# Optimization experiments

Measured on AMD Instinct MI355X. Metric: run time of the kernel, lower is better.

## Reference

```python
import jax, jax.numpy as jnp
import numpy as np

NUM_GRAPHS = 32

def leaky(x):
    return jax.nn.leaky_relu(x, 0.1)

def setup_inputs() -> dict:
    key = jax.random.key(0)
    ks = jax.random.split(key, 32)
    N, E = 8000, 32000
    x = jax.random.normal(ks[0], (N, 4), dtype=jnp.float32)
    edge_index = jax.random.randint(ks[1], (2, E), 0, N, dtype=jnp.int32)
    batch_index = jnp.sort(jax.random.randint(ks[2], (N,), 0, NUM_GRAPHS, dtype=jnp.int32))
    def lin(k, i, o, s=0.1):
        k1, k2 = jax.random.split(k)
        return jax.random.normal(k1, (i, o), dtype=jnp.float32) * s, jax.random.normal(k2, (o,), dtype=jnp.float32) * s
    p = {}
    # edge networks: Linear(3,64)+LeakyReLU+Linear(64, in*out)+LeakyReLU
    p['en1_w1'], p['en1_b1'] = lin(ks[3], 3, 64)
    p['en1_w2'], p['en1_b2'] = lin(ks[4], 64, 4 * 8)
    p['en2_w1'], p['en2_b1'] = lin(ks[5], 3, 64)
    p['en2_w2'], p['en2_b2'] = lin(ks[6], 64, 8 * 64)
    p['en3_w1'], p['en3_b1'] = lin(ks[7], 3, 64)
    p['en3_w2'], p['en3_b2'] = lin(ks[8], 64, 64 * 128)
    # NNConv root weights + biases
    p['root1'], p['cb1'] = lin(ks[9], 4, 8)
    p['root2'], p['cb2'] = lin(ks[10], 8, 64)
    p['root3'], p['cb3'] = lin(ks[11], 64, 128)
    # readout MLP
    p['fc1_w'], p['fc1_b'] = lin(ks[12], 128, 128)
    p['fc2_w'], p['fc2_b'] = lin(ks[13], 128, 64)
    p['fc3_w'], p['fc3_b'] = lin(ks[14], 64, 1)
    return dict(x=x, edge_index=edge_index, batch_index=batch_index, **p)

def nnconv(h, edge_index, edge_attr, w1, b1, w2, b2, root, cbias, in_ch, out_ch):
    # per-edge weight matrix from edge attributes
    e = leaky(edge_attr @ w1 + b1)              # [E,64]
    W = leaky(e @ w2 + b2).reshape(-1, in_ch, out_ch)  # [E,in,out]
    msg = jnp.einsum('ei,eio->eo', h[edge_index[0]], W)  # gather + per-edge matmul
    agg = jax.ops.segment_sum(msg, edge_index[1], num_segments=h.shape[0])  # scatter-add
    return agg + h @ root + cbias

def reference(x, edge_index, batch_index, en1_w1, en1_b1, en1_w2, en1_b2, en2_w1, en2_b1, en2_w2, en2_b2, en3_w1, en3_b1, en3_w2, en3_b2, root1, cb1, root2, cb2, root3, cb3, fc1_w, fc1_b, fc2_w, fc2_b, fc3_w, fc3_b):
    edge_attr = (x[edge_index[1]] - x[edge_index[0]])[:, 1:]  # [E,3] relative position
    h = leaky(nnconv(x, edge_index, edge_attr, en1_w1, en1_b1, en1_w2, en1_b2, root1, cb1, 4, 8))
    h = leaky(nnconv(h, edge_index, edge_attr, en2_w1, en2_b1, en2_w2, en2_b2, root2, cb2, 8, 64))
    h = leaky(nnconv(h, edge_index, edge_attr, en3_w1, en3_b1, en3_w2, en3_b2, root3, cb3, 64, 128))
    g = jax.ops.segment_sum(h, batch_index, num_segments=NUM_GRAPHS)  # sum-pool per graph
    g = leaky(g @ fc1_w + fc1_b)
    g = leaky(g @ fc2_w + fc2_b)
    return g @ fc3_w + fc3_b  # [G,1] total energies
```

## Files before the change

### kernel.cpp

```cpp
#include <hip/hip_runtime.h>
#include <hip/hip_bf16.h>

typedef __attribute__((ext_vector_type(8))) short short8;
typedef __attribute__((ext_vector_type(4))) float floatx4;

__device__ __forceinline__ float leaky(float v){ return v > 0.f ? v : 0.1f*v; }
__device__ __forceinline__ void atomAdd(float* p, float v){ unsafeAtomicAdd(p, v); }
__device__ __forceinline__ short f2bf(float f){
  __hip_bfloat16 h = __float2bfloat16(f);
  return *reinterpret_cast<short*>(&h);
}

__global__ void efeat_all(const float* __restrict__ x, const int* __restrict__ ei,
                          const float* __restrict__ w1a, const float* __restrict__ b1a,
                          const float* __restrict__ w1b, const float* __restrict__ b1b,
                          const float* __restrict__ w1c, const float* __restrict__ b1c,
                          float* __restrict__ ef1, short* __restrict__ ef2b,
                          short* __restrict__ ef3b, int E, int Epad){
  int id = blockIdx.x*256 + threadIdx.x;
  if (id >= Epad*64) return;
  int e = id >> 6, j = id & 63;
  if (e >= E){ ef1[id] = 0.f; ef2b[id] = 0; ef3b[id] = 0; return; }
  int s = ei[e], d = ei[E+e];
  float a0 = x[d*4+1] - x[s*4+1];
  float a1 = x[d*4+2] - x[s*4+2];
  float a2 = x[d*4+3] - x[s*4+3];
  float v1 = leaky(a0*w1a[j] + a1*w1a[64+j] + a2*w1a[128+j] + b1a[j]);
  float v2 = leaky(a0*w1b[j] + a1*w1b[64+j] + a2*w1b[128+j] + b1b[j]);
  float v3 = leaky(a0*w1c[j] + a1*w1c[64+j] + a2*w1c[128+j] + b1c[j]);
  ef1[id] = v1;
  ef2b[id] = f2bf(v2);
  ef3b[id] = f2bf(v3);
}

__global__ void pack_w2_all(const float* __restrict__ w2a, short* __restrict__ pa,
                            const float* __restrict__ w2b, short* __restrict__ pb){
  int bid = blockIdx.x;
  const float* w2; short* dst; int IC, OC, cbase;
  if (bid < 16){ w2 = w2a; dst = pa; IC = 8;  OC = 64;  cbase = bid*4; }
  else        { w2 = w2b; dst = pb; IC = 64; OC = 128; cbase = (bid-16)*4; }
  int lane = threadIdx.x & 63;
  int c = cbase + (threadIdx.x >> 6);
  int OT = OC/16;
  int kh = c & 1; int rem = c >> 1; int otg = rem % OT; int i = rem / OT;
  int n = lane & 15, q = lane >> 4;
  short out[8];
  #pragma unroll
  for (int j=0;j<8;j++){
    int k = kh*32 + q*8 + j;
    out[j] = f2bf(w2[(size_t)k*(IC*OC) + i*OC + otg*16 + n]);
  }
  *reinterpret_cast<short8*>(dst + (size_t)c*512 + lane*8) = *reinterpret_cast<short8*>(out);
}

__global__ void conv1_kernel(const float* __restrict__ ef, const float* __restrict__ x,
                             const int* __restrict__ ei, const float* __restrict__ w2,
                             const float* __restrict__ b2, float* __restrict__ agg, int E){
  int id = blockIdx.x*256 + threadIdx.x;
  if (id >= E*8) return;
  int e = id >> 3, o = id & 7;
  int s = ei[e], d = ei[E+e];
  const float* efe = ef + (size_t)e*64;
  float z[4];
  #pragma unroll
  for (int i=0;i<4;i++) z[i] = b2[i*8+o];
  for (int k=0;k<64;k++){
    float a = efe[k];
    #pragma unroll
    for (int i=0;i<4;i++) z[i] += a*w2[k*32 + i*8 + o];
  }
  float msg = 0.f;
  #pragma unroll
  for (int i=0;i<4;i++) msg += x[s*4+i]*leaky(z[i]);
  atomAdd(&agg[d*8+o], msg);
}

template<int IC, int OC>
__global__ void node_kernel(float* __restrict__ h, const float* __restrict__ hin,
                            const float* __restrict__ root, const float* __restrict__ cb, int N){
  int id = blockIdx.x*256 + threadIdx.x;
  if (id >= N*OC) return;
  int n = id / OC, o = id % OC;
  float v = h[id] + cb[o];
  const float* hi = hin + (size_t)n*IC;
  #pragma unroll
  for (int i=0;i<IC;i++) v += hi[i]*root[i*OC+o];
  h[id] = leaky(v);
}

__global__ void node3_pool(const float* __restrict__ agg, const float* __restrict__ hin,
                           const float* __restrict__ root, const float* __restrict__ cb,
                           const int* __restrict__ batch, float* __restrict__ g, int N){
  int id = blockIdx.x*256 + threadIdx.x;
  if (id >= N*128) return;
  int n = id >> 7, o = id & 127;
  float v = agg[id] + cb[o];
  const float* hi = hin + (size_t)n*64;
  #pragma unroll
  for (int i=0;i<64;i++) v += hi[i]*root[i*128+o];
  atomAdd(&g[batch[n]*128 + o], leaky(v));
}

template<int IC, int OC, int MB, int ICB>
__global__ __launch_bounds__(256)
void conv_mfma(const short* __restrict__ efb, const float* __restrict__ h,
               const int* __restrict__ ei, const short* __restrict__ w2p,
               const float* __restrict__ b2, float* __restrict__ agg, int E){
  constexpr int ME   = MB*16;
  constexpr int OT   = OC/16;
  constexpr int WOT  = OT/4;
  constexpr int NSPL = IC/ICB;
  __shared__ float hsT[ICB][ME];
  __shared__ int sdst[ME];
  int tid = threadIdx.x;
  int bi = blockIdx.x;
  int eb = (bi / NSPL) * ME;
  int i0 = (bi % NSPL) * ICB;

  {
    int e = tid % ME;
    int ge = eb + e;
    bool valid = ge < E;
    int src = valid ? ei[ge] : 0;
    constexpr int CH  = 256/ME;
    constexpr int IPC = ICB/CH;
    int c = tid / ME;
    const float* hp = h + (size_t)src*IC + i0 + c*IPC;
    if constexpr (IPC == 8){
      #pragma unroll
      for (int half=0; half<2; half++){
        float4 hv = valid ? reinterpret_cast<const float4*>(hp)[half]
                          : float4{0.f,0.f,0.f,0.f};
        hsT[c*IPC + half*4 + 0][e] = hv.x;
        hsT[c*IPC + half*4 + 1][e] = hv.y;
        hsT[c*IPC + half*4 + 2][e] = hv.z;
        hsT[c*IPC + half*4 + 3][e] = hv.w;
      }
    } else {
      #pragma unroll
      for (int j=0;j<IPC;j++)
        hsT[c*IPC + j][e] = valid ? hp[j] : 0.f;
    }
    if (tid < ME) sdst[tid] = (eb + tid < E) ? ei[E + eb + tid] : -1;
  }
  __syncthreads();

  int lane = tid & 63;
  int wv = tid >> 6;
  int n = lane & 15, quad = lane >> 4;
  int o0 = wv * (OC/4);

  short8 A[MB][2];
  #pragma unroll
  for (int m=0;m<MB;m++)
    #pragma unroll
    for (int kh=0;kh<2;kh++)
      A[m][kh] = *reinterpret_cast<const short8*>(efb + (size_t)(eb + m*16 + n)*64 + kh*32 + quad*8);

  float msg[MB][WOT][4];
  #pragma unroll
  for (int m=0;m<MB;m++)
    #pragma unroll
    for (int t=0;t<WOT;t++)
      #pragma unroll
      for (int r=0;r<4;r++) msg[m][t][r] = 0.f;

  for (int i=0;i<ICB;i++){
    int ig = i0 + i;
    short8 B[WOT][2];
    float bz[WOT];
    #pragma unroll
    for (int t=0;t<WOT;t++){
      int otg = (o0 >> 4) + t;
      #pragma unroll
      for (int kh=0;kh<2;kh++)
        B[t][kh] = *reinterpret_cast<const short8*>(w2p + ((size_t)((ig*OT + otg)*2 + kh) << 9) + lane*8);
      bz[t] = b2[ig*OC + o0 + t*16 + n];
    }
    #pragma unroll
    for (int m=0;m<MB;m++){
      float4 hv = *reinterpret_cast<const float4*>(&hsT[i][m*16 + quad*4]);
      #pragma unroll
      for (int t=0;t<WOT;t++){
        floatx4 z = {bz[t], bz[t], bz[t], bz[t]};
        z = __builtin_amdgcn_mfma_f32_16x16x32_bf16(A[m][0], B[t][0], z, 0, 0, 0);
        z = __builtin_amdgcn_mfma_f32_16x16x32_bf16(A[m][1], B[t][1], z, 0, 0, 0);
        float l0 = fmaxf(z[0], 0.1f*z[0]);
        float l1 = fmaxf(z[1], 0.1f*z[1]);
        float l2 = fmaxf(z[2], 0.1f*z[2]);
        float l3 = fmaxf(z[3], 0.1f*z[3]);
        msg[m][t][0] += hv.x*l0;
        msg[m][t][1] += hv.y*l1;
        msg[m][t][2] += hv.z*l2;
        msg[m][t][3] += hv.w*l3;
      }
    }
  }

  #pragma unroll
  for (int m=0;m<MB;m++){
    #pragma unroll
    for (int r=0;r<4;r++){
      int d = sdst[m*16 + quad*4 + r];
      if (d >= 0){
        #pragma unroll
        for (int t=0;t<WOT;t++)
          atomAdd(&agg[(size_t)d*OC + o0 + t*16 + n], msg[m][t][r]);
      }
    }
  }
}

__global__ void head_kernel(const float* __restrict__ g,
                            const float* __restrict__ fc1w, const float* __restrict__ fc1b,
                            const float* __restrict__ fc2w, const float* __restrict__ fc2b,
                            const float* __restrict__ fc3w, const float* __restrict__ fc3b,
                            float* __restrict__ out){
  __shared__ float s1[128], s2[128];
  int gi = blockIdx.x, t = threadIdx.x;
  s1[t] = g[gi*128+t];
  __syncthreads();
  float v = fc1b[t];
  for (int i=0;i<128;i++) v += s1[i]*fc1w[i*128+t];
  s2[t] = leaky(v);
  __syncthreads();
  if (t < 64){
    float v2 = fc2b[t];
    for (int i=0;i<128;i++) v2 += s2[i]*fc2w[i*64+t];
    s1[t] = leaky(v2);
  }
  __syncthreads();
  if (t == 0){
    float v3 = fc3b[0];
    for (int i=0;i<64;i++) v3 += s1[i]*fc3w[i];
    out[gi] = v3;
  }
}

extern "C" void kernel_launch(void* const* d_in, const int* in_sizes, int n_in,
                              void* d_out, int out_size, void* d_ws, size_t ws_size,
                              hipStream_t stream) {
  const float* x      = (const float*)d_in[0];
  const int*   ei     = (const int*)  d_in[1];
  const int*   batch  = (const int*)  d_in[2];
  const float* en1_w1 = (const float*)d_in[3];  const float* en1_b1 = (const float*)d_in[4];
  const float* en1_w2 = (const float*)d_in[5];  const float* en1_b2 = (const float*)d_in[6];
  const float* en2_w1 = (const float*)d_in[7];  const float* en2_b1 = (const float*)d_in[8];
  const float* en2_w2 = (const float*)d_in[9];  const float* en2_b2 = (const float*)d_in[10];
  const float* en3_w1 = (const float*)d_in[11]; const float* en3_b1 = (const float*)d_in[12];
  const float* en3_w2 = (const float*)d_in[13]; const float* en3_b2 = (const float*)d_in[14];
  const float* root1  = (const float*)d_in[15]; const float* cb1    = (const float*)d_in[16];
  const float* root2  = (const float*)d_in[17]; const float* cb2    = (const float*)d_in[18];
  const float* root3  = (const float*)d_in[19]; const float* cb3    = (const float*)d_in[20];
  const float* fc1w   = (const float*)d_in[21]; const float* fc1b   = (const float*)d_in[22];
  const float* fc2w   = (const float*)d_in[23]; const float* fc2b   = (const float*)d_in[24];
  const float* fc3w   = (const float*)d_in[25]; const float* fc3b   = (const float*)d_in[26];
  float* out = (float*)d_out;

  const int N = in_sizes[0] / 4;
  const int E = in_sizes[1] / 2;
  const int G = 32;
  const int Epad = (E + 63) & ~63;

  float* ef1  = (float*)d_ws;
  short* ef2b = (short*)(ef1 + (size_t)Epad*64);
  short* ef3b = ef2b + (size_t)Epad*64;
  short* w2p2 = ef3b + (size_t)Epad*64;
  short* w2p3 = w2p2 + 8*4*2*512;
  float* a1   = (float*)(w2p3 + 64*8*2*512);
  float* a2   = a1 + (size_t)N*8;
  float* a3   = a2 + (size_t)N*64;
  float* g    = a3 + (size_t)N*128;

  size_t zero_bytes = ((size_t)N*(8+64+128) + (size_t)G*128) * sizeof(float);
  hipMemsetAsync(a1, 0, zero_bytes, stream);

  efeat_all<<<(Epad*64 + 255)/256, 256, 0, stream>>>(
      x, ei, en1_w1, en1_b1, en2_w1, en2_b1, en3_w1, en3_b1,
      ef1, ef2b, ef3b, E, Epad);

  pack_w2_all<<<272, 256, 0, stream>>>(en2_w2, w2p2, en3_w2, w2p3);

  conv1_kernel<<<(E*8 + 255)/256, 256, 0, stream>>>(ef1, x, ei, en1_w2, en1_b2, a1, E);
  node_kernel<4,8><<<(N*8 + 255)/256, 256, 0, stream>>>(a1, x, root1, cb1, N);

  conv_mfma<8,64,2,8><<<Epad/32, 256, 0, stream>>>(ef2b, a1, ei, w2p2, en2_b2, a2, E);
  node_kernel<8,64><<<(N*64 + 255)/256, 256, 0, stream>>>(a2, a1, root2, cb2, N);

  conv_mfma<64,128,4,32><<<(Epad/64)*2, 256, 0, stream>>>(ef3b, a2, ei, w2p3, en3_b2, a3, E);
  node3_pool<<<(N*128 + 255)/256, 256, 0, stream>>>(a3, a2, root3, cb3, batch, g, N);

  head_kernel<<<G, 128, 0, stream>>>(g, fc1w, fc1b, fc2w, fc2b, fc3w, fc3b, out);
}
```

Before: 254.1 us.

## Fuse conv1 into edge-feature kernel, tile node3 pool, prefetch B in conv_mfma

Merges the conv1 message computation into the edge-feature kernel, keeping layer-1 edge features in shared memory and dropping the fp32 ef1 buffer and one launch. node3_pool now stages root3 and 16 node rows in LDS and accumulates per-graph partial sums before issuing atomics, which cuts the number of global atomics. conv_mfma double-buffers the B-fragment loads across the input-channel loop so they overlap with the MFMA work. The fused conv1 leaves only 32 of 256 threads busy in its second phase, and each node3 block reloads the full 32KB root matrix.

```diff
diff --git a/kernel.cpp b/kernel.cpp
--- a/kernel.cpp
+++ b/kernel.cpp
@@ -11,26 +11,51 @@
   return *reinterpret_cast<short*>(&h);
 }
 
-__global__ void efeat_all(const float* __restrict__ x, const int* __restrict__ ei,
-                          const float* __restrict__ w1a, const float* __restrict__ b1a,
-                          const float* __restrict__ w1b, const float* __restrict__ b1b,
-                          const float* __restrict__ w1c, const float* __restrict__ b1c,
-                          float* __restrict__ ef1, short* __restrict__ ef2b,
-                          short* __restrict__ ef3b, int E, int Epad){
-  int id = blockIdx.x*256 + threadIdx.x;
-  if (id >= Epad*64) return;
+__global__ void efeat_conv1(const float* __restrict__ x, const int* __restrict__ ei,
+                            const float* __restrict__ w1a, const float* __restrict__ b1a,
+                            const float* __restrict__ w1b, const float* __restrict__ b1b,
+                            const float* __restrict__ w1c, const float* __restrict__ b1c,
+                            const float* __restrict__ c1w2, const float* __restrict__ c1b2,
+                            short* __restrict__ ef2b, short* __restrict__ ef3b,
+                            float* __restrict__ agg1, int E, int Epad){
+  __shared__ float sm[4][64];
+  int tid = threadIdx.x;
+  int id = blockIdx.x*256 + tid;
   int e = id >> 6, j = id & 63;
-  if (e >= E){ ef1[id] = 0.f; ef2b[id] = 0; ef3b[id] = 0; return; }
-  int s = ei[e], d = ei[E+e];
-  float a0 = x[d*4+1] - x[s*4+1];
-  float a1 = x[d*4+2] - x[s*4+2];
-  float a2 = x[d*4+3] - x[s*4+3];
-  float v1 = leaky(a0*w1a[j] + a1*w1a[64+j] + a2*w1a[128+j] + b1a[j]);
-  float v2 = leaky(a0*w1b[j] + a1*w1b[64+j] + a2*w1b[128+j] + b1b[j]);
-  float v3 = leaky(a0*w1c[j] + a1*w1c[64+j] + a2*w1c[128+j] + b1c[j]);
-  ef1[id] = v1;
-  ef2b[id] = f2bf(v2);
-  ef3b[id] = f2bf(v3);
+  float v1 = 0.f;
+  if (e < Epad){
+    if (e >= E){ ef2b[id] = 0; ef3b[id] = 0; }
+    else {
+      int s = ei[e], d = ei[E+e];
+      float a0 = x[d*4+1] - x[s*4+1];
+      float a1 = x[d*4+2] - x[s*4+2];
+      float a2 = x[d*4+3] - x[s*4+3];
+      v1 = leaky(a0*w1a[j] + a1*w1a[64+j] + a2*w1a[128+j] + b1a[j]);
+      ef2b[id] = f2bf(leaky(a0*w1b[j] + a1*w1b[64+j] + a2*w1b[128+j] + b1b[j]));
+      ef3b[id] = f2bf(leaky(a0*w1c[j] + a1*w1c[64+j] + a2*w1c[128+j] + b1c[j]));
+    }
+  }
+  sm[tid >> 6][j] = v1;
+  __syncthreads();
+  if (tid < 32){
+    int le = tid >> 3, o = tid & 7;
+    int ge = blockIdx.x*4 + le;
+    if (ge < E){
+      int s = ei[ge], d = ei[E+ge];
+      float z[4];
+      #pragma unroll
+      for (int i=0;i<4;i++) z[i] = c1b2[i*8+o];
+      for (int k=0;k<64;k++){
+        float a = sm[le][k];
+        #pragma unroll
+        for (int i=0;i<4;i++) z[i] += a*c1w2[k*32 + i*8 + o];
+      }
+      float msg = 0.f;
+      #pragma unroll
+      for (int i=0;i<4;i++) msg += x[s*4+i]*leaky(z[i]);
+      atomAdd(&agg1[d*8+o], msg);
+    }
+  }
 }
 
 __global__ void pack_w2_all(const float* __restrict__ w2a, short* __restrict__ pa,
@@ -53,28 +78,6 @@
   *reinterpret_cast<short8*>(dst + (size_t)c*512 + lane*8) = *reinterpret_cast<short8*>(out);
 }
 
-__global__ void conv1_kernel(const float* __restrict__ ef, const float* __restrict__ x,
-                             const int* __restrict__ ei, const float* __restrict__ w2,
-                             const float* __restrict__ b2, float* __restrict__ agg, int E){
-  int id = blockIdx.x*256 + threadIdx.x;
-  if (id >= E*8) return;
-  int e = id >> 3, o = id & 7;
-  int s = ei[e], d = ei[E+e];
-  const float* efe = ef + (size_t)e*64;
-  float z[4];
-  #pragma unroll
-  for (int i=0;i<4;i++) z[i] = b2[i*8+o];
-  for (int k=0;k<64;k++){
-    float a = efe[k];
-    #pragma unroll
-    for (int i=0;i<4;i++) z[i] += a*w2[k*32 + i*8 + o];
-  }
-  float msg = 0.f;
-  #pragma unroll
-  for (int i=0;i<4;i++) msg += x[s*4+i]*leaky(z[i]);
-  atomAdd(&agg[d*8+o], msg);
-}
-
 template<int IC, int OC>
 __global__ void node_kernel(float* __restrict__ h, const float* __restrict__ hin,
                             const float* __restrict__ root, const float* __restrict__ cb, int N){
@@ -88,17 +91,40 @@
   h[id] = leaky(v);
 }
 
-__global__ void node3_pool(const float* __restrict__ agg, const float* __restrict__ hin,
-                           const float* __restrict__ root, const float* __restrict__ cb,
-                           const int* __restrict__ batch, float* __restrict__ g, int N){
-  int id = blockIdx.x*256 + threadIdx.x;
-  if (id >= N*128) return;
-  int n = id >> 7, o = id & 127;
-  float v = agg[id] + cb[o];
-  const float* hi = hin + (size_t)n*64;
-  #pragma unroll
-  for (int i=0;i<64;i++) v += hi[i]*root[i*128+o];
-  atomAdd(&g[batch[n]*128 + o], leaky(v));
+__global__ __launch_bounds__(256)
+void node3_pool(const float* __restrict__ agg, const float* __restrict__ hin,
+                const float* __restrict__ root, const float* __restrict__ cb,
+                const int* __restrict__ batch, float* __restrict__ g, int N){
+  __shared__ float rootS[64*128];
+  __shared__ float hrow[16][64];
+  int t = threadIdx.x;
+  #pragma unroll
+  for (int r=0;r<8;r++){
+    int idx = t + r*256;
+    reinterpret_cast<float4*>(rootS)[idx] = reinterpret_cast<const float4*>(root)[idx];
+  }
+  int n0 = blockIdx.x*16;
+  {
+    int nn = t >> 4, c = (t & 15)*4;
+    int n = n0 + nn;
+    float4 hv = (n < N) ? *reinterpret_cast<const float4*>(hin + (size_t)n*64 + c)
+                        : float4{0.f,0.f,0.f,0.f};
+    hrow[nn][c+0]=hv.x; hrow[nn][c+1]=hv.y; hrow[nn][c+2]=hv.z; hrow[nn][c+3]=hv.w;
+  }
+  __syncthreads();
+  int o = t & 127, np = t >> 7;
+  float acc = 0.f; int cur = -1;
+  for (int rep=0; rep<8; rep++){
+    int nl = rep*2 + np; int n = n0 + nl;
+    if (n >= N) break;
+    int b = batch[n];
+    if (b != cur){ if (cur >= 0) atomAdd(&g[cur*128+o], acc); acc = 0.f; cur = b; }
+    float v = agg[(size_t)n*128 + o] + cb[o];
+    #pragma unroll 16
+    for (int i=0;i<64;i++) v += hrow[nl][i]*rootS[i*128+o];
+    acc += leaky(v);
+  }
+  if (cur >= 0) atomAdd(&g[cur*128+o], acc);
 }
 
 template<int IC, int OC, int MB, int ICB>
@@ -165,26 +191,26 @@
       #pragma unroll
       for (int r=0;r<4;r++) msg[m][t][r] = 0.f;
 
-  for (int i=0;i<ICB;i++){
+  auto loadB = [&](int i, short8 (&Bt)[WOT][2], float (&bzt)[WOT]){
     int ig = i0 + i;
-    short8 B[WOT][2];
-    float bz[WOT];
     #pragma unroll
     for (int t=0;t<WOT;t++){
       int otg = (o0 >> 4) + t;
       #pragma unroll
       for (int kh=0;kh<2;kh++)
-        B[t][kh] = *reinterpret_cast<const short8*>(w2p + ((size_t)((ig*OT + otg)*2 + kh) << 9) + lane*8);
-      bz[t] = b2[ig*OC + o0 + t*16 + n];
-    }
+        Bt[t][kh] = *reinterpret_cast<const short8*>(w2p + ((size_t)((ig*OT + otg)*2 + kh) << 9) + lane*8);
+      bzt[t] = b2[ig*OC + o0 + t*16 + n];
+    }
+  };
+  auto compute = [&](int i, short8 (&Bt)[WOT][2], float (&bzt)[WOT]){
     #pragma unroll
     for (int m=0;m<MB;m++){
       float4 hv = *reinterpret_cast<const float4*>(&hsT[i][m*16 + quad*4]);
       #pragma unroll
       for (int t=0;t<WOT;t++){
-        floatx4 z = {bz[t], bz[t], bz[t], bz[t]};
-        z = __builtin_amdgcn_mfma_f32_16x16x32_bf16(A[m][0], B[t][0], z, 0, 0, 0);
-        z = __builtin_amdgcn_mfma_f32_16x16x32_bf16(A[m][1], B[t][1], z, 0, 0, 0);
+        floatx4 z = {bzt[t], bzt[t], bzt[t], bzt[t]};
+        z = __builtin_amdgcn_mfma_f32_16x16x32_bf16(A[m][0], Bt[t][0], z, 0, 0, 0);
+        z = __builtin_amdgcn_mfma_f32_16x16x32_bf16(A[m][1], Bt[t][1], z, 0, 0, 0);
         float l0 = fmaxf(z[0], 0.1f*z[0]);
         float l1 = fmaxf(z[1], 0.1f*z[1]);
         float l2 = fmaxf(z[2], 0.1f*z[2]);
@@ -195,7 +221,20 @@
         msg[m][t][3] += hv.w*l3;
       }
     }
-  }
+  };
+
+  short8 Bc[WOT][2], Bn[WOT][2];
+  float bzc[WOT], bzn[WOT];
+  loadB(0, Bc, bzc);
+  for (int i=0;i<ICB-1;i++){
+    loadB(i+1, Bn, bzn);
+    compute(i, Bc, bzc);
+    #pragma unroll
+    for (int t=0;t<WOT;t++){
+      Bc[t][0] = Bn[t][0]; Bc[t][1] = Bn[t][1]; bzc[t] = bzn[t];
+    }
+  }
+  compute(ICB-1, Bc, bzc);
 
   #pragma unroll
   for (int m=0;m<MB;m++){
@@ -262,8 +301,7 @@
   const int G = 32;
   const int Epad = (E + 63) & ~63;
 
-  float* ef1  = (float*)d_ws;
-  short* ef2b = (short*)(ef1 + (size_t)Epad*64);
+  short* ef2b = (short*)d_ws;
   short* ef3b = ef2b + (size_t)Epad*64;
   short* w2p2 = ef3b + (size_t)Epad*64;
   short* w2p3 = w2p2 + 8*4*2*512;
@@ -275,20 +313,19 @@
   size_t zero_bytes = ((size_t)N*(8+64+128) + (size_t)G*128) * sizeof(float);
   hipMemsetAsync(a1, 0, zero_bytes, stream);
 
-  efeat_all<<<(Epad*64 + 255)/256, 256, 0, stream>>>(
+  efeat_conv1<<<Epad/4, 256, 0, stream>>>(
       x, ei, en1_w1, en1_b1, en2_w1, en2_b1, en3_w1, en3_b1,
-      ef1, ef2b, ef3b, E, Epad);
+      en1_w2, en1_b2, ef2b, ef3b, a1, E, Epad);
 
   pack_w2_all<<<272, 256, 0, stream>>>(en2_w2, w2p2, en3_w2, w2p3);
 
-  conv1_kernel<<<(E*8 + 255)/256, 256, 0, stream>>>(ef1, x, ei, en1_w2, en1_b2, a1, E);
   node_kernel<4,8><<<(N*8 + 255)/256, 256, 0, stream>>>(a1, x, root1, cb1, N);
 
   conv_mfma<8,64,2,8><<<Epad/32, 256, 0, stream>>>(ef2b, a1, ei, w2p2, en2_b2, a2, E);
   node_kernel<8,64><<<(N*64 + 255)/256, 256, 0, stream>>>(a2, a1, root2, cb2, N);
 
   conv_mfma<64,128,4,32><<<(Epad/64)*2, 256, 0, stream>>>(ef3b, a2, ei, w2p3, en3_b2, a3, E);
-  node3_pool<<<(N*128 + 255)/256, 256, 0, stream>>>(a3, a2, root3, cb3, batch, g, N);
+  node3_pool<<<(N + 15)/16, 256, 0, stream>>>(a3, a2, root3, cb3, batch, g, N);
 
   head_kernel<<<G, 128, 0, stream>>>(g, fc1w, fc1b, fc2w, fc2b, fc3w, fc3b, out);
 }
```

Measured after the change: 247.5 us. -2.6%, faster.
